# Kernel optimization log

Hardware: AMD Instinct MI355X
Metric: run time of the kernel (lower is better)

The kernel has to match this reference:

```python
import jax, jax.numpy as jnp
import numpy as np

B, C, H, W = 8, 256, 64, 64
R = 8
CP = max(C // R, 3)  # C' = 32


def setup_inputs() -> dict:
    key = jax.random.key(0)
    ks = jax.random.split(key, 9)
    s_in = 1.0 / np.sqrt(C)
    s_cp = 1.0 / np.sqrt(CP)
    return {
        "x": jax.random.normal(ks[0], (B, C, H, W), dtype=jnp.float32),
        "Wq": jax.random.uniform(ks[1], (CP, C), minval=-s_in, maxval=s_in, dtype=jnp.float32),
        "bq": jax.random.uniform(ks[2], (CP,), minval=-s_in, maxval=s_in, dtype=jnp.float32),
        "Wk": jax.random.uniform(ks[3], (CP, C), minval=-s_in, maxval=s_in, dtype=jnp.float32),
        "bk": jax.random.uniform(ks[4], (CP,), minval=-s_in, maxval=s_in, dtype=jnp.float32),
        "Wv": jax.random.uniform(ks[5], (CP, C), minval=-s_in, maxval=s_in, dtype=jnp.float32),
        "bv": jax.random.uniform(ks[6], (CP,), minval=-s_in, maxval=s_in, dtype=jnp.float32),
        "Wb": jax.random.uniform(ks[7], (C, CP), minval=-s_cp, maxval=s_cp, dtype=jnp.float32),
        "bb": jax.random.uniform(ks[8], (C,), minval=-s_cp, maxval=s_cp, dtype=jnp.float32),
    }


def reference(x, Wq, bq, Wk, bk, Wv, bv, Wb, bb):
    b, c, h, w = x.shape
    n = h * w
    xf = x.reshape(b, c, n)  # [B, C, N]
    # 1x1 convs == channel-wise linear projections
    q = jnp.einsum('oc,bcn->bon', Wq, xf) + bq[None, :, None]  # [B, C', N]
    k = jnp.einsum('oc,bcn->bon', Wk, xf) + bk[None, :, None]
    v = jnp.einsum('oc,bcn->bon', Wv, xf) + bv[None, :, None]
    # attention: softmax(Q^T K) over last dim -> [B, N, N]
    attn = jax.nn.softmax(jnp.einsum('bon,bom->bnm', q, k), axis=-1)
    # out[b,c,i] = sum_j v[b,c,j] * attn[b,j,i]
    out = jnp.einsum('bcj,bji->bci', v, attn)  # [B, C', N]
    back = jnp.einsum('co,bon->bcn', Wb, out) + bb[None, :, None]  # [B, C, N]
    return back.reshape(b, c, h, w) + x
```

## Files before the change

kernel.cpp:

```cpp
#include <hip/hip_runtime.h>
#include <hip/hip_bf16.h>

#define NB 8
#define CC 256
#define CP 32
#define NN 4096
#define LOG2E 1.44269504088896340736f

typedef __attribute__((ext_vector_type(8))) short short8;
typedef __attribute__((ext_vector_type(4))) float floatx4;
typedef __attribute__((ext_vector_type(4))) int intx4;

static __device__ __forceinline__ ushort bf16r(float f) {
    __hip_bfloat16 h = __float2bfloat16(f);
    return *reinterpret_cast<ushort*>(&h);
}
static __device__ __forceinline__ float bf2f(ushort u) {
    union { unsigned int i; float f; } x;
    x.i = ((unsigned int)u) << 16;
    return x.f;
}
static __device__ __forceinline__ short8 load_frag(const ushort* p) {
    intx4 v = *reinterpret_cast<const intx4*>(p);
    return *reinterpret_cast<short8*>(&v);
}
static __device__ __forceinline__ unsigned int pk2(float a, float b) {
#if defined(__has_builtin) && __has_builtin(__builtin_amdgcn_perm)
    return __builtin_amdgcn_perm(__float_as_uint(b) + 0x8000u, __float_as_uint(a) + 0x8000u, 0x07060302u);
#else
    unsigned int ua = __float_as_uint(a) + 0x8000u;
    unsigned int ub = __float_as_uint(b) + 0x8000u;
    return (ua >> 16) | (ub & 0xFFFF0000u);
#endif
}
static __device__ __forceinline__ ushort pk1(float a) {
    return (ushort)((__float_as_uint(a) + 0x8000u) >> 16);
}
static __device__ __forceinline__ float fexp2(float x) {
#if defined(__has_builtin)
#if __has_builtin(__builtin_amdgcn_exp2f)
    return __builtin_amdgcn_exp2f(x);
#else
    return __expf(x * 0.69314718055994530942f);
#endif
#else
    return __expf(x * 0.69314718055994530942f);
#endif
}

__global__ void prep_w(const float* __restrict__ Wq, const float* __restrict__ Wk,
                       const float* __restrict__ Wv, const float* __restrict__ Wb,
                       ushort* __restrict__ W96, ushort* __restrict__ W2b) {
    int r = blockIdx.x, c = threadIdx.x;
    if (r < 96) {
        const float* src = (r < 32) ? (Wq + r * CC) : ((r < 64) ? (Wk + (r - 32) * CC) : (Wv + (r - 64) * CC));
        float scale = (r < 32) ? LOG2E : 1.0f;
        W96[r * CC + c] = bf16r(src[c] * scale);
    } else {
        int idx = (r - 96) * 256 + c;
        W2b[idx] = bf16r(Wb[idx]);
    }
}

__global__ __launch_bounds__(256) void proj_kernel(
    const float* __restrict__ x, const ushort* __restrict__ W96,
    const float* __restrict__ bq, const float* __restrict__ bk, const float* __restrict__ bv,
    ushort* __restrict__ Qt, ushort* __restrict__ Kt, ushort* __restrict__ Vt) {
    __shared__ ushort xt[64 * 264];
    int b = blockIdx.x >> 6, nt = blockIdx.x & 63;
    int t = threadIdx.x;
    int n0 = nt * 64;
    {
        int cq = t >> 4, n4 = (t & 15) * 4;
#pragma unroll
        for (int cc = 0; cc < 4; cc++) {
            int c_base = cc * 64 + cq * 4;
            float4 xv[4];
#pragma unroll
            for (int e = 0; e < 4; e++)
                xv[e] = *reinterpret_cast<const float4*>(&x[((size_t)b * CC + c_base + e) * NN + n0 + n4]);
            const float* xs = reinterpret_cast<const float*>(xv);
#pragma unroll
            for (int jj = 0; jj < 4; jj++) {
                ushort4 u;
                u.x = pk1(xs[0 * 4 + jj]);
                u.y = pk1(xs[1 * 4 + jj]);
                u.z = pk1(xs[2 * 4 + jj]);
                u.w = pk1(xs[3 * 4 + jj]);
                *reinterpret_cast<ushort4*>(&xt[(n4 + jj) * 264 + c_base]) = u;
            }
        }
    }
    __syncthreads();
    int w = t >> 6, lane = t & 63, l15 = lane & 15, q = lane >> 4;
    floatx4 acc[6];
#pragma unroll
    for (int k = 0; k < 6; k++) acc[k] = (floatx4){0.f, 0.f, 0.f, 0.f};
#pragma unroll
    for (int ks = 0; ks < 8; ks++) {
        short8 bfrag = load_frag(&xt[(w * 16 + l15) * 264 + ks * 32 + q * 8]);
#pragma unroll
        for (int ot = 0; ot < 6; ot++) {
            short8 afrag = load_frag(&W96[(size_t)(ot * 16 + l15) * CC + ks * 32 + q * 8]);
            acc[ot] = __builtin_amdgcn_mfma_f32_16x16x32_bf16(afrag, bfrag, acc[ot], 0, 0, 0);
        }
    }
    int n = n0 + w * 16 + l15;
#pragma unroll
    for (int ot = 0; ot < 6; ot++) {
        const float* bias = (ot < 2) ? bq : ((ot < 4) ? bk : bv);
        ushort* dst = (ot < 2) ? Qt : ((ot < 4) ? Kt : Vt);
        int o0 = (ot & 1) * 16 + q * 4;
        float4 b4 = *reinterpret_cast<const float4*>(bias + o0);
        float sc = (ot < 2) ? LOG2E : 1.0f;
        ushort4 pk;
        pk.x = bf16r(acc[ot][0] + b4.x * sc);
        pk.y = bf16r(acc[ot][1] + b4.y * sc);
        pk.z = bf16r(acc[ot][2] + b4.z * sc);
        pk.w = bf16r(acc[ot][3] + b4.w * sc);
        *reinterpret_cast<ushort4*>(&dst[((size_t)b * NN + n) * CP + o0]) = pk;
    }
}

__global__ __launch_bounds__(256, 6) void passA_kernel(
    const ushort* __restrict__ Qt, const ushort* __restrict__ Kt, float* __restrict__ Fp) {
    __shared__ float red[4][64];
    int bid = blockIdx.x;
    int mq = bid & 3, jt = (bid >> 2) & 63, b = bid >> 8;
    int w = threadIdx.x >> 6, lane = threadIdx.x & 63;
    int l15 = lane & 15, q = lane >> 4;

    short8 af[4];
#pragma unroll
    for (int js = 0; js < 4; js++)
        af[js] = load_frag(&Qt[((size_t)b * NN + jt * 64 + js * 16 + l15) * CP + q * 8]);

    floatx4 lacc[4];
#pragma unroll
    for (int js = 0; js < 4; js++) lacc[js] = (floatx4){0.f, 0.f, 0.f, 0.f};

    const ushort* kbase = Kt + ((size_t)b * NN + mq * 1024 + w * 256 + l15) * CP + q * 8;
    short8 bfc = load_frag(kbase);

#pragma unroll 2
    for (int ms = 0; ms < 16; ms++) {
        int mn = (ms + 1) & 15;
        short8 bfn = load_frag(kbase + (size_t)(mn * 16) * CP);
        floatx4 z = (floatx4){0.f, 0.f, 0.f, 0.f};
#pragma unroll
        for (int js = 0; js < 4; js++) {
            floatx4 s = __builtin_amdgcn_mfma_f32_16x16x32_bf16(af[js], bfc, z, 0, 0, 0);
            lacc[js][0] += fexp2(s[0]);
            lacc[js][1] += fexp2(s[1]);
            lacc[js][2] += fexp2(s[2]);
            lacc[js][3] += fexp2(s[3]);
        }
        bfc = bfn;
    }
#pragma unroll
    for (int js = 0; js < 4; js++) {
#pragma unroll
        for (int d = 1; d < 16; d <<= 1) {
            lacc[js][0] += __shfl_xor(lacc[js][0], d, 64);
            lacc[js][1] += __shfl_xor(lacc[js][1], d, 64);
            lacc[js][2] += __shfl_xor(lacc[js][2], d, 64);
            lacc[js][3] += __shfl_xor(lacc[js][3], d, 64);
        }
    }
    if (l15 == 0) {
#pragma unroll
        for (int js = 0; js < 4; js++) {
#pragma unroll
            for (int r = 0; r < 4; r++) red[w][js * 16 + q * 4 + r] = lacc[js][r];
        }
    }
    __syncthreads();
    int t = threadIdx.x;
    if (t < 64) {
        float s = red[0][t] + red[1][t] + red[2][t] + red[3][t];
        Fp[((size_t)mq * NB + b) * NN + jt * 64 + t] = s;
    }
}

__global__ __launch_bounds__(256) void fold_kernel(
    const ushort* __restrict__ Vt, const float* __restrict__ Fp, ushort* __restrict__ Vp) {
    __shared__ ushort tile[32 * 136];
    const size_t PL = (size_t)NB * NN;
    int b = blockIdx.x >> 5, nc = blockIdx.x & 31;
    int t = threadIdx.x;
    int half = t >> 7, nl = t & 127;
    int n = nc * 128 + nl;
    size_t bn = (size_t)b * NN + n;
    float f = 1.0f / (Fp[bn] + Fp[PL + bn] + Fp[2 * PL + bn] + Fp[3 * PL + bn]);
    const ushort* src = &Vt[bn * CP + half * 16];
#pragma unroll
    for (int g = 0; g < 2; g++) {
        intx4 raw = *reinterpret_cast<const intx4*>(src + g * 8);
        const ushort* us = reinterpret_cast<const ushort*>(&raw);
#pragma unroll
        for (int e = 0; e < 8; e++) {
            tile[(half * 16 + g * 8 + e) * 136 + nl] = pk1(bf2f(us[e]) * f);
        }
    }
    __syncthreads();
#pragma unroll
    for (int cc = 0; cc < 16; cc++) {
        int c = half * 16 + cc;
        Vp[((size_t)b * CP + c) * NN + nc * 128 + nl] = tile[c * 136 + nl];
    }
}

__global__ __launch_bounds__(256, 4) void passB_kernel(
    const ushort* __restrict__ Qt, const ushort* __restrict__ Kt, const ushort* __restrict__ Vp,
    const ushort* __restrict__ W2b, const float* __restrict__ bb, const float* __restrict__ x,
    float* __restrict__ out) {
    __shared__ float olds4[4 * 32 * 33];

    int bid = blockIdx.x;
    int it = bid & 127, b = bid >> 7;
    int w = threadIdx.x >> 6, lane = threadIdx.x & 63;
    int l15 = lane & 15, q = lane >> 4;
    int i0 = it * 32;

    short8 kf0 = load_frag(&Kt[((size_t)b * NN + i0 + l15) * CP + q * 8]);
    short8 kf1 = load_frag(&Kt[((size_t)b * NN + i0 + 16 + l15) * CP + q * 8]);

    floatx4 acc00 = (floatx4){0.f, 0.f, 0.f, 0.f};
    floatx4 acc10 = (floatx4){0.f, 0.f, 0.f, 0.f};
    floatx4 acc01 = (floatx4){0.f, 0.f, 0.f, 0.f};
    floatx4 acc11 = (floatx4){0.f, 0.f, 0.f, 0.f};

    int qrow = (l15 >> 2) * 8 + (l15 & 3);
    const ushort* qbase = Qt + ((size_t)b * NN + qrow) * CP + q * 8;
    const ushort* vbase0 = Vp + ((size_t)b * CP + l15) * NN + q * 8;
    const ushort* vbase1 = Vp + ((size_t)b * CP + 16 + l15) * NN + q * 8;

    int jf = w * 32;
    short8 a0c = load_frag(qbase + (size_t)jf * CP);
    short8 a1c = load_frag(qbase + (size_t)(jf + 4) * CP);
    short8 va0c = load_frag(vbase0 + jf);
    short8 va1c = load_frag(vbase1 + jf);

#pragma unroll 2
    for (int jb = w; jb < 128; jb += 4) {
        int jn0 = ((jb + 4) & 127) * 32;
        short8 a0n = load_frag(qbase + (size_t)jn0 * CP);
        short8 a1n = load_frag(qbase + (size_t)(jn0 + 4) * CP);
        short8 va0n = load_frag(vbase0 + jn0);
        short8 va1n = load_frag(vbase1 + jn0);

        floatx4 z = (floatx4){0.f, 0.f, 0.f, 0.f};
        floatx4 s0A = __builtin_amdgcn_mfma_f32_16x16x32_bf16(a0c, kf0, z, 0, 0, 0);
        floatx4 s1A = __builtin_amdgcn_mfma_f32_16x16x32_bf16(a1c, kf0, z, 0, 0, 0);
        floatx4 s0B = __builtin_amdgcn_mfma_f32_16x16x32_bf16(a0c, kf1, z, 0, 0, 0);
        floatx4 s1B = __builtin_amdgcn_mfma_f32_16x16x32_bf16(a1c, kf1, z, 0, 0, 0);

        union { intx4 v; short8 s; } wa, wb2;
        wa.v.x = pk2(fexp2(s0A[0]), fexp2(s0A[1]));
        wa.v.y = pk2(fexp2(s0A[2]), fexp2(s0A[3]));
        wa.v.z = pk2(fexp2(s1A[0]), fexp2(s1A[1]));
        wa.v.w = pk2(fexp2(s1A[2]), fexp2(s1A[3]));
        wb2.v.x = pk2(fexp2(s0B[0]), fexp2(s0B[1]));
        wb2.v.y = pk2(fexp2(s0B[2]), fexp2(s0B[3]));
        wb2.v.z = pk2(fexp2(s1B[0]), fexp2(s1B[1]));
        wb2.v.w = pk2(fexp2(s1B[2]), fexp2(s1B[3]));

        acc00 = __builtin_amdgcn_mfma_f32_16x16x32_bf16(va0c, wa.s, acc00, 0, 0, 0);
        acc10 = __builtin_amdgcn_mfma_f32_16x16x32_bf16(va1c, wa.s, acc10, 0, 0, 0);
        acc01 = __builtin_amdgcn_mfma_f32_16x16x32_bf16(va0c, wb2.s, acc01, 0, 0, 0);
        acc11 = __builtin_amdgcn_mfma_f32_16x16x32_bf16(va1c, wb2.s, acc11, 0, 0, 0);

        a0c = a0n; a1c = a1n; va0c = va0n; va1c = va1n;
    }

    int mbase = w * (32 * 33);
#pragma unroll
    for (int r = 0; r < 4; r++) {
        olds4[mbase + (q * 4 + r) * 33 + l15] = acc00[r];
        olds4[mbase + (16 + q * 4 + r) * 33 + l15] = acc10[r];
        olds4[mbase + (q * 4 + r) * 33 + 16 + l15] = acc01[r];
        olds4[mbase + (16 + q * 4 + r) * 33 + 16 + l15] = acc11[r];
    }
    __syncthreads();

    short8 bfr[2];
#pragma unroll
    for (int s = 0; s < 2; s++) {
        float o8[8];
#pragma unroll
        for (int jj = 0; jj < 8; jj++) {
            int o = q * 8 + jj;
            int idx = o * 33 + s * 16 + l15;
            o8[jj] = olds4[idx] + olds4[1056 + idx] + olds4[2112 + idx] + olds4[3168 + idx];
        }
        union { intx4 v; short8 sh; } u;
        u.v.x = pk2(o8[0], o8[1]);
        u.v.y = pk2(o8[2], o8[3]);
        u.v.z = pk2(o8[4], o8[5]);
        u.v.w = pk2(o8[6], o8[7]);
        bfr[s] = u.sh;
    }
    int c0 = w * 64;
#pragma unroll
    for (int cs = 0; cs < 4; cs++) {
        short8 af = load_frag(&W2b[(size_t)(c0 + cs * 16 + l15) * CP + q * 8]);
#pragma unroll
        for (int s = 0; s < 2; s++) {
            floatx4 z = (floatx4){0.f, 0.f, 0.f, 0.f};
            floatx4 d = __builtin_amdgcn_mfma_f32_16x16x32_bf16(af, bfr[s], z, 0, 0, 0);
#pragma unroll
            for (int r = 0; r < 4; r++) {
                int c = c0 + cs * 16 + q * 4 + r;
                int i = i0 + s * 16 + l15;
                size_t idx = ((size_t)b * CC + c) * NN + i;
                out[idx] = d[r] + bb[c] + x[idx];
            }
        }
    }
}

extern "C" void kernel_launch(void* const* d_in, const int* in_sizes, int n_in,
                              void* d_out, int out_size, void* d_ws, size_t ws_size,
                              hipStream_t stream) {
    const float* x  = (const float*)d_in[0];
    const float* Wq = (const float*)d_in[1];
    const float* bq = (const float*)d_in[2];
    const float* Wk = (const float*)d_in[3];
    const float* bk = (const float*)d_in[4];
    const float* Wv = (const float*)d_in[5];
    const float* bv = (const float*)d_in[6];
    const float* Wb = (const float*)d_in[7];
    const float* bb = (const float*)d_in[8];
    float* out = (float*)d_out;

    char* ws = (char*)d_ws;
    ushort* Qt  = (ushort*)(ws);
    ushort* Kt  = (ushort*)(ws + (2u << 20));
    ushort* Vp  = (ushort*)(ws + (4u << 20));
    ushort* Vt  = (ushort*)(ws + (6u << 20));
    float*  Fp  = (float*) (ws + (8u << 20));
    ushort* W96 = (ushort*)(ws + (8u << 20) + (1u << 19));
    ushort* W2b = (ushort*)(ws + (8u << 20) + (1u << 19) + (48u << 10));

    prep_w<<<128, 256, 0, stream>>>(Wq, Wk, Wv, Wb, W96, W2b);
    proj_kernel<<<512, 256, 0, stream>>>(x, W96, bq, bk, bv, Qt, Kt, Vt);
    passA_kernel<<<2048, 256, 0, stream>>>(Qt, Kt, Fp);
    fold_kernel<<<256, 256, 0, stream>>>(Vt, Fp, Vp);
    passB_kernel<<<1024, 256, 0, stream>>>(Qt, Kt, Vp, W2b, bb, x, out);
}
```

Before: 180.3 us.

## Stage K/Q/V tiles through LDS double buffers and write V transposed directly

The projection kernel now writes V straight into the channel-major Vp layout, so the fold kernel scales Vp in place with vectorized loads instead of transposing from Vt through shared memory. Pass A now splits the key range in two per block instead of four, halving the grid. Pass A and pass B stage K, or Q and V, tiles through per-wave double-buffered LDS with coalesced 16-byte global loads, replacing the strided fragment loads straight from global memory. The cost is more LDS traffic and a larger shared footprint per block, which may limit occupancy. The per-wave buffers carry no barrier inside the loop, so their correctness relies on each wave's own LDS accesses being ordered.

Measured after the change: 163.4 us. -9.4%, faster.

```diff
diff --git a/kernel.cpp b/kernel.cpp
--- a/kernel.cpp
+++ b/kernel.cpp
@@ -65,7 +65,7 @@
 __global__ __launch_bounds__(256) void proj_kernel(
     const float* __restrict__ x, const ushort* __restrict__ W96,
     const float* __restrict__ bq, const float* __restrict__ bk, const float* __restrict__ bv,
-    ushort* __restrict__ Qt, ushort* __restrict__ Kt, ushort* __restrict__ Vt) {
+    ushort* __restrict__ Qt, ushort* __restrict__ Kt, ushort* __restrict__ Vp) {
     __shared__ ushort xt[64 * 264];
     int b = blockIdx.x >> 6, nt = blockIdx.x & 63;
     int t = threadIdx.x;
@@ -107,9 +107,9 @@
     }
     int n = n0 + w * 16 + l15;
 #pragma unroll
-    for (int ot = 0; ot < 6; ot++) {
-        const float* bias = (ot < 2) ? bq : ((ot < 4) ? bk : bv);
-        ushort* dst = (ot < 2) ? Qt : ((ot < 4) ? Kt : Vt);
+    for (int ot = 0; ot < 4; ot++) {
+        const float* bias = (ot < 2) ? bq : bk;
+        ushort* dst = (ot < 2) ? Qt : Kt;
         int o0 = (ot & 1) * 16 + q * 4;
         float4 b4 = *reinterpret_cast<const float4*>(bias + o0);
         float sc = (ot < 2) ? LOG2E : 1.0f;
@@ -120,13 +120,24 @@
         pk.w = bf16r(acc[ot][3] + b4.w * sc);
         *reinterpret_cast<ushort4*>(&dst[((size_t)b * NN + n) * CP + o0]) = pk;
     }
-}
-
-__global__ __launch_bounds__(256, 6) void passA_kernel(
+#pragma unroll
+    for (int ot = 4; ot < 6; ot++) {
+        int o0 = ((ot - 4) & 1) * 16 + q * 4;
+        float4 b4 = *reinterpret_cast<const float4*>(bv + o0);
+        const float* av = reinterpret_cast<const float*>(&acc[ot]);
+        const float* bvv = reinterpret_cast<const float*>(&b4);
+#pragma unroll
+        for (int r = 0; r < 4; r++) {
+            Vp[((size_t)b * CP + o0 + r) * NN + n] = bf16r(av[r] + bvv[r]);
+        }
+    }
+}
+
+__global__ __launch_bounds__(256, 4) void passA_kernel(
     const ushort* __restrict__ Qt, const ushort* __restrict__ Kt, float* __restrict__ Fp) {
-    __shared__ float red[4][64];
+    __shared__ __align__(16) ushort smem[20480];
     int bid = blockIdx.x;
-    int mq = bid & 3, jt = (bid >> 2) & 63, b = bid >> 8;
+    int mq = bid & 1, jt = (bid >> 1) & 63, b = bid >> 7;
     int w = threadIdx.x >> 6, lane = threadIdx.x & 63;
     int l15 = lane & 15, q = lane >> 4;
 
@@ -139,24 +150,49 @@
 #pragma unroll
     for (int js = 0; js < 4; js++) lacc[js] = (floatx4){0.f, 0.f, 0.f, 0.f};
 
-    const ushort* kbase = Kt + ((size_t)b * NN + mq * 1024 + w * 256 + l15) * CP + q * 8;
-    short8 bfc = load_frag(kbase);
+    const ushort* Kb = Kt + (size_t)b * NN * CP;
+    int mbase = mq * 2048 + w * 512;
+    ushort* wbase = smem + w * 5120;
+    int r1 = lane >> 2, p8 = (lane & 3) * 8;
+
+    {
+        int m0 = mbase;
+#pragma unroll
+        for (int s = 0; s < 4; s++) {
+            int row = r1 + 16 * s;
+            intx4 v = *reinterpret_cast<const intx4*>(Kb + (size_t)(m0 + row) * CP + p8);
+            *reinterpret_cast<intx4*>(wbase + row * 40 + p8) = v;
+        }
+    }
 
 #pragma unroll 2
-    for (int ms = 0; ms < 16; ms++) {
-        int mn = (ms + 1) & 15;
-        short8 bfn = load_frag(kbase + (size_t)(mn * 16) * CP);
-        floatx4 z = (floatx4){0.f, 0.f, 0.f, 0.f};
-#pragma unroll
-        for (int js = 0; js < 4; js++) {
-            floatx4 s = __builtin_amdgcn_mfma_f32_16x16x32_bf16(af[js], bfc, z, 0, 0, 0);
-            lacc[js][0] += fexp2(s[0]);
-            lacc[js][1] += fexp2(s[1]);
-            lacc[js][2] += fexp2(s[2]);
-            lacc[js][3] += fexp2(s[3]);
-        }
-        bfc = bfn;
-    }
+    for (int t = 0; t < 8; t++) {
+        int mn = mbase + ((t + 1) & 7) * 64;
+        intx4 nk[4];
+#pragma unroll
+        for (int s = 0; s < 4; s++)
+            nk[s] = *reinterpret_cast<const intx4*>(Kb + (size_t)(mn + r1 + 16 * s) * CP + p8);
+
+        ushort* cb = wbase + (t & 1) * 2560;
+#pragma unroll
+        for (int ms = 0; ms < 4; ms++) {
+            short8 bf = load_frag(cb + (ms * 16 + l15) * 40 + q * 8);
+            floatx4 z = (floatx4){0.f, 0.f, 0.f, 0.f};
+#pragma unroll
+            for (int js = 0; js < 4; js++) {
+                floatx4 s = __builtin_amdgcn_mfma_f32_16x16x32_bf16(af[js], bf, z, 0, 0, 0);
+                lacc[js][0] += fexp2(s[0]);
+                lacc[js][1] += fexp2(s[1]);
+                lacc[js][2] += fexp2(s[2]);
+                lacc[js][3] += fexp2(s[3]);
+            }
+        }
+        ushort* nb = wbase + ((t + 1) & 1) * 2560;
+#pragma unroll
+        for (int s = 0; s < 4; s++)
+            *reinterpret_cast<intx4*>(nb + (r1 + 16 * s) * 40 + p8) = nk[s];
+    }
+
 #pragma unroll
     for (int js = 0; js < 4; js++) {
 #pragma unroll
@@ -167,46 +203,44 @@
             lacc[js][3] += __shfl_xor(lacc[js][3], d, 64);
         }
     }
+    __syncthreads();
+    float* red = reinterpret_cast<float*>(smem);
     if (l15 == 0) {
 #pragma unroll
         for (int js = 0; js < 4; js++) {
 #pragma unroll
-            for (int r = 0; r < 4; r++) red[w][js * 16 + q * 4 + r] = lacc[js][r];
+            for (int r = 0; r < 4; r++) red[w * 64 + js * 16 + q * 4 + r] = lacc[js][r];
         }
     }
     __syncthreads();
     int t = threadIdx.x;
     if (t < 64) {
-        float s = red[0][t] + red[1][t] + red[2][t] + red[3][t];
+        float s = red[t] + red[64 + t] + red[128 + t] + red[192 + t];
         Fp[((size_t)mq * NB + b) * NN + jt * 64 + t] = s;
     }
 }
 
 __global__ __launch_bounds__(256) void fold_kernel(
-    const ushort* __restrict__ Vt, const float* __restrict__ Fp, ushort* __restrict__ Vp) {
-    __shared__ ushort tile[32 * 136];
+    ushort* __restrict__ Vp, const float* __restrict__ Fp) {
     const size_t PL = (size_t)NB * NN;
-    int b = blockIdx.x >> 5, nc = blockIdx.x & 31;
+    int b = blockIdx.x >> 4, sl = blockIdx.x & 15;
     int t = threadIdx.x;
-    int half = t >> 7, nl = t & 127;
-    int n = nc * 128 + nl;
-    size_t bn = (size_t)b * NN + n;
-    float f = 1.0f / (Fp[bn] + Fp[PL + bn] + Fp[2 * PL + bn] + Fp[3 * PL + bn]);
-    const ushort* src = &Vt[bn * CP + half * 16];
-#pragma unroll
-    for (int g = 0; g < 2; g++) {
-        intx4 raw = *reinterpret_cast<const intx4*>(src + g * 8);
+    int nn = sl * 256 + (t & 31) * 8;
+    int cg = t >> 5;
+    size_t bn = (size_t)b * NN + nn;
+    float f[8];
+#pragma unroll
+    for (int e = 0; e < 8; e++) f[e] = 1.0f / (Fp[bn + e] + Fp[PL + bn + e]);
+#pragma unroll
+    for (int r = 0; r < 4; r++) {
+        int c = cg * 4 + r;
+        ushort* p = Vp + ((size_t)b * CP + c) * NN + nn;
+        intx4 raw = *reinterpret_cast<const intx4*>(p);
         const ushort* us = reinterpret_cast<const ushort*>(&raw);
-#pragma unroll
-        for (int e = 0; e < 8; e++) {
-            tile[(half * 16 + g * 8 + e) * 136 + nl] = pk1(bf2f(us[e]) * f);
-        }
-    }
-    __syncthreads();
-#pragma unroll
-    for (int cc = 0; cc < 16; cc++) {
-        int c = half * 16 + cc;
-        Vp[((size_t)b * CP + c) * NN + nc * 128 + nl] = tile[c * 136 + nl];
+        ushort o[8];
+#pragma unroll
+        for (int e = 0; e < 8; e++) o[e] = pk1(bf2f(us[e]) * f[e]);
+        *reinterpret_cast<intx4*>(p) = *reinterpret_cast<intx4*>(o);
     }
 }
 
@@ -214,7 +248,7 @@
     const ushort* __restrict__ Qt, const ushort* __restrict__ Kt, const ushort* __restrict__ Vp,
     const ushort* __restrict__ W2b, const float* __restrict__ bb, const float* __restrict__ x,
     float* __restrict__ out) {
-    __shared__ float olds4[4 * 32 * 33];
+    __shared__ __align__(16) ushort smem[20480];
 
     int bid = blockIdx.x;
     int it = bid & 127, b = bid >> 7;
@@ -231,29 +265,42 @@
     floatx4 acc11 = (floatx4){0.f, 0.f, 0.f, 0.f};
 
     int qrow = (l15 >> 2) * 8 + (l15 & 3);
-    const ushort* qbase = Qt + ((size_t)b * NN + qrow) * CP + q * 8;
-    const ushort* vbase0 = Vp + ((size_t)b * CP + l15) * NN + q * 8;
-    const ushort* vbase1 = Vp + ((size_t)b * CP + 16 + l15) * NN + q * 8;
-
-    int jf = w * 32;
-    short8 a0c = load_frag(qbase + (size_t)jf * CP);
-    short8 a1c = load_frag(qbase + (size_t)(jf + 4) * CP);
-    short8 va0c = load_frag(vbase0 + jf);
-    short8 va1c = load_frag(vbase1 + jf);
+    const ushort* Qb = Qt + (size_t)b * NN * CP;
+    const ushort* Vb = Vp + (size_t)b * CP * NN;
+    ushort* wbase = smem + w * 5120;
+    int r1 = lane >> 2, p8 = (lane & 3) * 8;
+
+    {
+        int j0 = w * 32;
+        intx4 q1 = *reinterpret_cast<const intx4*>(Qb + (size_t)(j0 + r1) * CP + p8);
+        intx4 q2 = *reinterpret_cast<const intx4*>(Qb + (size_t)(j0 + r1 + 16) * CP + p8);
+        intx4 v1 = *reinterpret_cast<const intx4*>(Vb + (size_t)r1 * NN + j0 + p8);
+        intx4 v2 = *reinterpret_cast<const intx4*>(Vb + (size_t)(r1 + 16) * NN + j0 + p8);
+        *reinterpret_cast<intx4*>(wbase + r1 * 40 + p8) = q1;
+        *reinterpret_cast<intx4*>(wbase + (r1 + 16) * 40 + p8) = q2;
+        *reinterpret_cast<intx4*>(wbase + 1280 + r1 * 40 + p8) = v1;
+        *reinterpret_cast<intx4*>(wbase + 1280 + (r1 + 16) * 40 + p8) = v2;
+    }
 
 #pragma unroll 2
-    for (int jb = w; jb < 128; jb += 4) {
-        int jn0 = ((jb + 4) & 127) * 32;
-        short8 a0n = load_frag(qbase + (size_t)jn0 * CP);
-        short8 a1n = load_frag(qbase + (size_t)(jn0 + 4) * CP);
-        short8 va0n = load_frag(vbase0 + jn0);
-        short8 va1n = load_frag(vbase1 + jn0);
+    for (int t = 0; t < 32; t++) {
+        int jn = ((w + (t + 1) * 4) & 127) * 32;
+        intx4 nq1 = *reinterpret_cast<const intx4*>(Qb + (size_t)(jn + r1) * CP + p8);
+        intx4 nq2 = *reinterpret_cast<const intx4*>(Qb + (size_t)(jn + r1 + 16) * CP + p8);
+        intx4 nv1 = *reinterpret_cast<const intx4*>(Vb + (size_t)r1 * NN + jn + p8);
+        intx4 nv2 = *reinterpret_cast<const intx4*>(Vb + (size_t)(r1 + 16) * NN + jn + p8);
+
+        ushort* cb = wbase + (t & 1) * 2560;
+        short8 a0 = load_frag(cb + qrow * 40 + q * 8);
+        short8 a1 = load_frag(cb + (qrow + 4) * 40 + q * 8);
+        short8 va0 = load_frag(cb + 1280 + l15 * 40 + q * 8);
+        short8 va1 = load_frag(cb + 1280 + (16 + l15) * 40 + q * 8);
 
         floatx4 z = (floatx4){0.f, 0.f, 0.f, 0.f};
-        floatx4 s0A = __builtin_amdgcn_mfma_f32_16x16x32_bf16(a0c, kf0, z, 0, 0, 0);
-        floatx4 s1A = __builtin_amdgcn_mfma_f32_16x16x32_bf16(a1c, kf0, z, 0, 0, 0);
-        floatx4 s0B = __builtin_amdgcn_mfma_f32_16x16x32_bf16(a0c, kf1, z, 0, 0, 0);
-        floatx4 s1B = __builtin_amdgcn_mfma_f32_16x16x32_bf16(a1c, kf1, z, 0, 0, 0);
+        floatx4 s0A = __builtin_amdgcn_mfma_f32_16x16x32_bf16(a0, kf0, z, 0, 0, 0);
+        floatx4 s1A = __builtin_amdgcn_mfma_f32_16x16x32_bf16(a1, kf0, z, 0, 0, 0);
+        floatx4 s0B = __builtin_amdgcn_mfma_f32_16x16x32_bf16(a0, kf1, z, 0, 0, 0);
+        floatx4 s1B = __builtin_amdgcn_mfma_f32_16x16x32_bf16(a1, kf1, z, 0, 0, 0);
 
         union { intx4 v; short8 s; } wa, wb2;
         wa.v.x = pk2(fexp2(s0A[0]), fexp2(s0A[1]));
@@ -265,14 +312,20 @@
         wb2.v.z = pk2(fexp2(s1B[0]), fexp2(s1B[1]));
         wb2.v.w = pk2(fexp2(s1B[2]), fexp2(s1B[3]));
 
-        acc00 = __builtin_amdgcn_mfma_f32_16x16x32_bf16(va0c, wa.s, acc00, 0, 0, 0);
-        acc10 = __builtin_amdgcn_mfma_f32_16x16x32_bf16(va1c, wa.s, acc10, 0, 0, 0);
-        acc01 = __builtin_amdgcn_mfma_f32_16x16x32_bf16(va0c, wb2.s, acc01, 0, 0, 0);
-        acc11 = __builtin_amdgcn_mfma_f32_16x16x32_bf16(va1c, wb2.s, acc11, 0, 0, 0);
-
-        a0c = a0n; a1c = a1n; va0c = va0n; va1c = va1n;
-    }
-
+        acc00 = __builtin_amdgcn_mfma_f32_16x16x32_bf16(va0, wa.s, acc00, 0, 0, 0);
+        acc10 = __builtin_amdgcn_mfma_f32_16x16x32_bf16(va1, wa.s, acc10, 0, 0, 0);
+        acc01 = __builtin_amdgcn_mfma_f32_16x16x32_bf16(va0, wb2.s, acc01, 0, 0, 0);
+        acc11 = __builtin_amdgcn_mfma_f32_16x16x32_bf16(va1, wb2.s, acc11, 0, 0, 0);
+
+        ushort* nb = wbase + ((t + 1) & 1) * 2560;
+        *reinterpret_cast<intx4*>(nb + r1 * 40 + p8) = nq1;
+        *reinterpret_cast<intx4*>(nb + (r1 + 16) * 40 + p8) = nq2;
+        *reinterpret_cast<intx4*>(nb + 1280 + r1 * 40 + p8) = nv1;
+        *reinterpret_cast<intx4*>(nb + 1280 + (r1 + 16) * 40 + p8) = nv2;
+    }
+
+    __syncthreads();
+    float* olds4 = reinterpret_cast<float*>(smem);
     int mbase = w * (32 * 33);
 #pragma unroll
     for (int r = 0; r < 4; r++) {
@@ -337,14 +390,13 @@
     ushort* Qt  = (ushort*)(ws);
     ushort* Kt  = (ushort*)(ws + (2u << 20));
     ushort* Vp  = (ushort*)(ws + (4u << 20));
-    ushort* Vt  = (ushort*)(ws + (6u << 20));
-    float*  Fp  = (float*) (ws + (8u << 20));
-    ushort* W96 = (ushort*)(ws + (8u << 20) + (1u << 19));
-    ushort* W2b = (ushort*)(ws + (8u << 20) + (1u << 19) + (48u << 10));
+    float*  Fp  = (float*) (ws + (6u << 20));
+    ushort* W96 = (ushort*)(ws + (6u << 20) + (1u << 19));
+    ushort* W2b = (ushort*)(ws + (6u << 20) + (1u << 19) + (48u << 10));
 
     prep_w<<<128, 256, 0, stream>>>(Wq, Wk, Wv, Wb, W96, W2b);
-    proj_kernel<<<512, 256, 0, stream>>>(x, W96, bq, bk, bv, Qt, Kt, Vt);
-    passA_kernel<<<2048, 256, 0, stream>>>(Qt, Kt, Fp);
-    fold_kernel<<<256, 256, 0, stream>>>(Vt, Fp, Vp);
+    proj_kernel<<<512, 256, 0, stream>>>(x, W96, bq, bk, bv, Qt, Kt, Vp);
+    passA_kernel<<<1024, 256, 0, stream>>>(Qt, Kt, Fp);
+    fold_kernel<<<128, 256, 0, stream>>>(Vp, Fp);
     passB_kernel<<<1024, 256, 0, stream>>>(Qt, Kt, Vp, W2b, bb, x, out);
 }
```
